# Kernel optimization log

Measured on AMD Instinct MI355X. Metric: run time of the kernel, lower is better.

The kernel has to match this reference:

```python
import jax, jax.numpy as jnp
import numpy as np

B, T, C, H = 4, 2048, 1024, 16
D = C // H  # head dim = 64


def setup_inputs() -> dict:
    key = jax.random.key(0)
    ks = jax.random.split(key, 5)
    s = 0.02
    return {
        "x": jax.random.normal(ks[0], (B, T, C), dtype=jnp.float32),
        "W_attn": jax.random.normal(ks[1], (C, 3 * C), dtype=jnp.float32) * s,
        "b_attn": jnp.zeros((3 * C,), dtype=jnp.float32),
        "W_proj": jax.random.normal(ks[2], (C, C), dtype=jnp.float32) * s,
        "b_proj": jnp.zeros((C,), dtype=jnp.float32),
    }


def reference(x, W_attn, b_attn, W_proj, b_proj):
    # qkv projection: [B,T,3C]
    qkv = x @ W_attn + b_attn
    q, k, v = jnp.split(qkv, 3, axis=-1)
    # [B,T,C] -> [B,H,T,D]
    def heads(t):
        return t.reshape(B, T, H, D).transpose(0, 2, 1, 3)
    q, k, v = heads(q), heads(k), heads(v)
    # scaled scores with causal mask, materialized [B,H,T,T] as in original
    att = jnp.einsum('bhqd,bhkd->bhqk', q, k) * (1.0 / np.sqrt(D))
    causal = jnp.tril(jnp.ones((T, T), dtype=bool))
    att = jnp.where(causal[None, None], att, -jnp.inf)
    att = jax.nn.softmax(att, axis=-1)
    y = jnp.einsum('bhqk,bhkd->bhqd', att, v)  # [B,H,T,D]
    y = y.transpose(0, 2, 1, 3).reshape(B, T, C)
    y = y @ W_proj + b_proj
    # original also returns present=(k,v); it is a pure pass-through cache
    return y
```

## Files before the change

kernel.cpp:

```cpp
#include <hip/hip_runtime.h>


typedef unsigned short u16;
typedef unsigned int u32;
typedef __attribute__((ext_vector_type(8))) unsigned short u16x8;
typedef __attribute__((ext_vector_type(4))) unsigned short u16x4;
typedef __attribute__((ext_vector_type(8))) short short8;
typedef __attribute__((ext_vector_type(4))) float f32x4;

__device__ inline u16 f2bf(float f) {
  unsigned u = __float_as_uint(f);
  u = (u + 0x7FFF + ((u >> 16) & 1)) >> 16;
  return (u16)u;
}

__device__ inline f32x4 mfma16(short8 a, short8 b, f32x4 c) {
  return __builtin_amdgcn_mfma_f32_16x16x32_bf16(a, b, c, 0, 0, 0);
}

__global__ __launch_bounds__(256) void k_cvt(const float* __restrict__ in,
                                             u16* __restrict__ out) {
  int i = (blockIdx.x * 256 + threadIdx.x) * 4;
  float4 v = *(const float4*)(in + i);
  u16x4 o = {f2bf(v.x), f2bf(v.y), f2bf(v.z), f2bf(v.w)};
  *(u16x4*)(out + i) = o;
}

__global__ __launch_bounds__(256) void k_tw(const float* __restrict__ in,
                                            u16* __restrict__ outT, int R, int Cc) {
  __shared__ u16 t[64][65];
  int c0 = blockIdx.x * 64, r0 = blockIdx.y * 64;
  int a = threadIdx.x & 63, w = threadIdx.x >> 6;
#pragma unroll
  for (int j = 0; j < 16; ++j) {
    int r = w + j * 4;
    t[r][a] = f2bf(in[(size_t)(r0 + r) * Cc + c0 + a]);
  }
  __syncthreads();
#pragma unroll
  for (int j = 0; j < 16; ++j) {
    int c = w + j * 4;
    outT[(size_t)(c0 + c) * R + r0 + a] = t[a][c];
  }
}

__global__ __launch_bounds__(256) void k_tv(const u16* __restrict__ qkv,
                                            u16* __restrict__ vt) {
  __shared__ u16 t[64][65];
  int t0 = blockIdx.x * 64, h = blockIdx.y, b = blockIdx.z;
  int a = threadIdx.x & 63, w = threadIdx.x >> 6;
#pragma unroll
  for (int j = 0; j < 16; ++j) {
    int tr = w + j * 4;
    t[tr][a] = qkv[(size_t)(b * 2048 + t0 + tr) * 3072 + 2048 + h * 64 + a];
  }
  __syncthreads();
#pragma unroll
  for (int j = 0; j < 16; ++j) {
    int d = w + j * 4;
    vt[((size_t)((b * 16 + h) * 64 + d)) * 2048 + t0 + a] = t[a][d];
  }
}

template <int OUTBF, int QSCALE>
__global__ __launch_bounds__(256) void gemm_bt(const u16* __restrict__ A,
                                               const u16* __restrict__ Bt,
                                               const float* __restrict__ bias,
                                               u16* __restrict__ outb,
                                               float* __restrict__ outf,
                                               int M, int N, int K) {
  __shared__ u16 As[128 * 64];
  __shared__ u16 Bs[128 * 64];
  const int m0 = blockIdx.x * 128, n0 = blockIdx.y * 128;
  const int tid = threadIdx.x, wave = tid >> 6, lane = tid & 63;
  const int quad = lane >> 4, l16 = lane & 15;
  const int wm = (wave & 1) * 64, wn = (wave >> 1) * 64;
  const int lrow = lane >> 3;
  const int lch = lane & 7;
  const int slot = lch ^ lrow;
  const u16* sA[4];
  const u16* sB[4];
  int offA[4], offB[4];
#pragma unroll
  for (int j = 0; j < 4; ++j) {
    int r = wave * 32 + j * 8;
    sA[j] = A + (size_t)(m0 + r + lrow) * K + lch * 8;
    sB[j] = Bt + (size_t)(n0 + r + lrow) * K + lch * 8;
    offA[j] = (r + lrow) * 64 + slot * 8;
    offB[j] = offA[j];
  }
  u16x8 ra[4], rb[4];
#pragma unroll
  for (int j = 0; j < 4; ++j) {
    ra[j] = *(const u16x8*)(sA[j]);
    rb[j] = *(const u16x8*)(sB[j]);
  }
  f32x4 acc[4][4] = {};
  for (int kt = 0; kt < K; kt += 64) {
    __syncthreads();
#pragma unroll
    for (int j = 0; j < 4; ++j) {
      *(u16x8*)&As[offA[j]] = ra[j];
      *(u16x8*)&Bs[offB[j]] = rb[j];
    }
    __syncthreads();
    if (kt + 64 < K) {
#pragma unroll
      for (int j = 0; j < 4; ++j) {
        ra[j] = *(const u16x8*)(sA[j] + kt + 64);
        rb[j] = *(const u16x8*)(sB[j] + kt + 64);
      }
    }
    const int sl = l16 & 7;
#pragma unroll
    for (int ks = 0; ks < 2; ++ks) {
      short8 af[4], bf[4];
#pragma unroll
      for (int mt = 0; mt < 4; ++mt)
        af[mt] = *(const short8*)(As + (wm + mt * 16 + l16) * 64 +
                                  ((ks * 4 + quad) ^ sl) * 8);
#pragma unroll
      for (int nt = 0; nt < 4; ++nt)
        bf[nt] = *(const short8*)(Bs + (wn + nt * 16 + l16) * 64 +
                                  ((ks * 4 + quad) ^ sl) * 8);
#pragma unroll
      for (int mt = 0; mt < 4; ++mt)
#pragma unroll
        for (int nt = 0; nt < 4; ++nt)
          acc[mt][nt] = mfma16(af[mt], bf[nt], acc[mt][nt]);
    }
  }
#pragma unroll
  for (int nt = 0; nt < 4; ++nt) {
    int col = n0 + wn + nt * 16 + l16;
    float bv = bias[col];
#pragma unroll
    for (int mt = 0; mt < 4; ++mt) {
      int rowb = m0 + wm + mt * 16 + quad * 4;
#pragma unroll
      for (int r = 0; r < 4; ++r) {
        float v = acc[mt][nt][r] + bv;
        if (QSCALE && col < 1024) v *= 0.18033688f;
        if (OUTBF)
          outb[(size_t)(rowb + r) * N + col] = f2bf(v);
        else
          outf[(size_t)(rowb + r) * N + col] = v;
      }
    }
  }
}

#define ATP 72
__global__ __launch_bounds__(256) void attn(const u16* __restrict__ qkv,
                                            const u16* __restrict__ vt,
                                            u16* __restrict__ y) {
  __shared__ u16 shm[256 * ATP];
  u16* Qs = shm;
  u16* Ks = shm + 128 * ATP;
  u16* Vs = shm + 192 * ATP;
  const int p = blockIdx.x, h = blockIdx.y, b = blockIdx.z;
  const int tid = threadIdx.x, wave = tid >> 6, lane = tid & 63;
  const int quad = lane >> 4, l16 = lane & 15;
  const u16* Qg = qkv + (size_t)b * 2048 * 3072 + h * 64;
  const u16* Kg = Qg + 1024;
  const u16* Vtg = vt + (size_t)(b * 16 + h) * 64 * 2048;
  const int srow0 = tid >> 3, scol0 = (tid & 7) * 8;
  u16* Pw0 = Qs + (wave * 16) * ATP;
  u16* Pw1 = Qs + (64 + wave * 16) * ATP;
  short8 ones_f;
#pragma unroll
  for (int j = 0; j < 8; ++j) ones_f[j] = 0x3F80;

  for (int half = 0; half < 2; ++half) {
    const int qb = half ? (15 - p) : p;
    const int q0 = qb * 128;
    const int nkt = 2 * qb + 2;
    const u16* kp0 = Kg + (size_t)srow0 * 3072 + scol0;
    const u16* kp1 = kp0 + 32 * 3072;
    const u16* vp0 = Vtg + (size_t)srow0 * 2048 + scol0;
    const u16* vp1 = vp0 + 32 * 2048;
    u16x8 qr0 = *(const u16x8*)(Qg + (size_t)(q0 + srow0) * 3072 + scol0);
    u16x8 qr1 = *(const u16x8*)(Qg + (size_t)(q0 + srow0 + 32) * 3072 + scol0);
    u16x8 qr2 = *(const u16x8*)(Qg + (size_t)(q0 + srow0 + 64) * 3072 + scol0);
    u16x8 qr3 = *(const u16x8*)(Qg + (size_t)(q0 + srow0 + 96) * 3072 + scol0);
    u16x8 kreg0 = *(const u16x8*)kp0, kreg1 = *(const u16x8*)kp1;
    u16x8 vreg0 = *(const u16x8*)vp0, vreg1 = *(const u16x8*)vp1;
    __syncthreads();
    *(u16x8*)&Qs[(size_t)srow0 * ATP + scol0] = qr0;
    *(u16x8*)&Qs[(size_t)(srow0 + 32) * ATP + scol0] = qr1;
    *(u16x8*)&Qs[(size_t)(srow0 + 64) * ATP + scol0] = qr2;
    *(u16x8*)&Qs[(size_t)(srow0 + 96) * ATP + scol0] = qr3;
    *(u16x8*)&Ks[(size_t)srow0 * ATP + scol0] = kreg0;
    *(u16x8*)&Ks[(size_t)(srow0 + 32) * ATP + scol0] = kreg1;
    *(u16x8*)&Vs[(size_t)srow0 * ATP + scol0] = vreg0;
    *(u16x8*)&Vs[(size_t)(srow0 + 32) * ATP + scol0] = vreg1;
    __syncthreads();
    short8 qf0a = *(const short8*)&Qs[(wave * 16 + l16) * ATP + quad * 8];
    short8 qf1a = *(const short8*)&Qs[(wave * 16 + l16) * ATP + 32 + quad * 8];
    short8 qf0b = *(const short8*)&Qs[(64 + wave * 16 + l16) * ATP + quad * 8];
    short8 qf1b = *(const short8*)&Qs[(64 + wave * 16 + l16) * ATP + 32 + quad * 8];

    f32x4 lacc0 = {}, lacc1 = {};
    f32x4 o0[4] = {}, o1[4] = {};

    auto tile = [&](int kt, int g0mode, bool g1mask) {
      if (kt > 0) {
        __syncthreads();
        *(u16x8*)&Ks[(size_t)srow0 * ATP + scol0] = kreg0;
        *(u16x8*)&Ks[(size_t)(srow0 + 32) * ATP + scol0] = kreg1;
        *(u16x8*)&Vs[(size_t)srow0 * ATP + scol0] = vreg0;
        *(u16x8*)&Vs[(size_t)(srow0 + 32) * ATP + scol0] = vreg1;
        __syncthreads();
      }
      if (kt + 1 < nkt) {
        kreg0 = *(const u16x8*)(kp0 += 64 * 3072);
        kreg1 = *(const u16x8*)(kp1 += 64 * 3072);
        vreg0 = *(const u16x8*)(vp0 += 64);
        vreg1 = *(const u16x8*)(vp1 += 64);
      }

      f32x4 s0[4] = {}, s1[4] = {};
#pragma unroll
      for (int mt = 0; mt < 4; ++mt) {
        short8 kf0 = *(const short8*)&Ks[(mt * 16 + l16) * ATP + quad * 8];
        short8 kf1 = *(const short8*)&Ks[(mt * 16 + l16) * ATP + 32 + quad * 8];
        if (g0mode < 2) {
          s0[mt] = mfma16(kf0, qf0a, s0[mt]);
          s0[mt] = mfma16(kf1, qf1a, s0[mt]);
        }
        s1[mt] = mfma16(kf0, qf0b, s1[mt]);
        s1[mt] = mfma16(kf1, qf1b, s1[mt]);
      }

      if (g0mode < 2) {
        const int qrow = q0 + wave * 16 + l16;
#pragma unroll
        for (int mt = 0; mt < 4; ++mt) {
          float pe[4];
#pragma unroll
          for (int r = 0; r < 4; ++r) {
            float pv = __builtin_amdgcn_exp2f(s0[mt][r]);
            if (g0mode == 1) {
              int kcol = kt * 64 + mt * 16 + quad * 4 + r;
              if (kcol > qrow) pv = 0.f;
            }
            pe[r] = pv;
          }
          u32 lo = __builtin_amdgcn_perm(__float_as_uint(pe[1]),
                                         __float_as_uint(pe[0]), 0x07060302u);
          u32 hi = __builtin_amdgcn_perm(__float_as_uint(pe[3]),
                                         __float_as_uint(pe[2]), 0x07060302u);
          uint2 pk = {lo, hi};
          *(uint2*)&Pw0[l16 * ATP + mt * 16 + quad * 4] = pk;
        }
      }
      {
        const int qrow = q0 + 64 + wave * 16 + l16;
#pragma unroll
        for (int mt = 0; mt < 4; ++mt) {
          float pe[4];
#pragma unroll
          for (int r = 0; r < 4; ++r) {
            float pv = __builtin_amdgcn_exp2f(s1[mt][r]);
            if (g1mask) {
              int kcol = kt * 64 + mt * 16 + quad * 4 + r;
              if (kcol > qrow) pv = 0.f;
            }
            pe[r] = pv;
          }
          u32 lo = __builtin_amdgcn_perm(__float_as_uint(pe[1]),
                                         __float_as_uint(pe[0]), 0x07060302u);
          u32 hi = __builtin_amdgcn_perm(__float_as_uint(pe[3]),
                                         __float_as_uint(pe[2]), 0x07060302u);
          uint2 pk = {lo, hi};
          *(uint2*)&Pw1[l16 * ATP + mt * 16 + quad * 4] = pk;
        }
      }

#pragma unroll
      for (int ks = 0; ks < 2; ++ks) {
        short8 pf0, pf1;
        if (g0mode < 2) {
          pf0 = *(const short8*)&Pw0[l16 * ATP + ks * 32 + quad * 8];
          lacc0 = mfma16(pf0, ones_f, lacc0);
        }
        pf1 = *(const short8*)&Pw1[l16 * ATP + ks * 32 + quad * 8];
        lacc1 = mfma16(pf1, ones_f, lacc1);
#pragma unroll
        for (int dt = 0; dt < 4; ++dt) {
          short8 vf = *(const short8*)&Vs[(dt * 16 + l16) * ATP + ks * 32 + quad * 8];
          if (g0mode < 2) o0[dt] = mfma16(pf0, vf, o0[dt]);
          o1[dt] = mfma16(pf1, vf, o1[dt]);
        }
      }
    };

    for (int kt = 0; kt < nkt - 2; ++kt) tile(kt, 0, false);
    tile(nkt - 2, 1, false);
    tile(nkt - 1, 2, true);

    size_t rb0 = (size_t)b * 2048 + q0 + wave * 16 + quad * 4;
#pragma unroll
    for (int r = 0; r < 4; ++r) {
      float inv = 1.f / lacc0[r];
#pragma unroll
      for (int dt = 0; dt < 4; ++dt)
        y[(rb0 + r) * 1024 + h * 64 + dt * 16 + l16] = f2bf(o0[dt][r] * inv);
    }
    size_t rb1 = rb0 + 64;
#pragma unroll
    for (int r = 0; r < 4; ++r) {
      float inv = 1.f / lacc1[r];
#pragma unroll
      for (int dt = 0; dt < 4; ++dt)
        y[(rb1 + r) * 1024 + h * 64 + dt * 16 + l16] = f2bf(o1[dt][r] * inv);
    }
  }
}

extern "C" void kernel_launch(void* const* d_in, const int* in_sizes, int n_in,
                              void* d_out, int out_size, void* d_ws, size_t ws_size,
                              hipStream_t stream) {
  const float* x = (const float*)d_in[0];
  const float* W_attn = (const float*)d_in[1];
  const float* b_attn = (const float*)d_in[2];
  const float* W_proj = (const float*)d_in[3];
  const float* b_proj = (const float*)d_in[4];
  float* out = (float*)d_out;
  char* ws = (char*)d_ws;
  u16* xb  = (u16*)(ws);
  u16* wta = (u16*)(ws + 16777216);
  u16* wtp = (u16*)(ws + 23068672);
  u16* qkv = (u16*)(ws + 25165824);
  u16* vt  = (u16*)(ws + 75497472);
  u16* y   = (u16*)(ws + 92274688);

  k_cvt<<<dim3(8192), 256, 0, stream>>>(x, xb);
  k_tw<<<dim3(48, 16), 256, 0, stream>>>(W_attn, wta, 1024, 3072);
  k_tw<<<dim3(16, 16), 256, 0, stream>>>(W_proj, wtp, 1024, 1024);
  gemm_bt<1, 1><<<dim3(64, 24), 256, 0, stream>>>(xb, wta, b_attn, qkv, nullptr, 8192, 3072, 1024);
  k_tv<<<dim3(32, 16, 4), 256, 0, stream>>>(qkv, vt);
  attn<<<dim3(8, 16, 4), 256, 0, stream>>>(qkv, vt, y);
  gemm_bt<0, 0><<<dim3(64, 8), 256, 0, stream>>>(y, wtp, b_proj, nullptr, out, 8192, 1024, 1024);
}
```

Before: 251.4 us.

## Replace QKV GEMM with 256x256 tile, 8-wave kernel using async LDS loads

Adds a new GEMM kernel for the QKV projection that uses 256x256 output tiles with 512 threads. It streams A and B directly into shared memory with global_load_lds through a 4-deep ring buffer, using swizzled columns to avoid LDS bank conflicts. MFMA phases are interleaved with barriers and priority raises. This targets global-to-LDS latency and register staging overhead and raises arithmetic intensity per tile. In exchange, the grid is smaller (384 blocks) and 128 KB of LDS per block limits occupancy, so tail effects could offset the gains.

```diff
diff --git a/kernel.cpp b/kernel.cpp
--- a/kernel.cpp
+++ b/kernel.cpp
@@ -18,6 +18,11 @@
   return __builtin_amdgcn_mfma_f32_16x16x32_bf16(a, b, c, 0, 0, 0);
 }
 
+__device__ __forceinline__ void gld16(const u16* g, u16* l) {
+  __builtin_amdgcn_global_load_lds((const __attribute__((address_space(1))) void*)g,
+                                   (__attribute__((address_space(3))) void*)l, 16, 0, 0);
+}
+
 __global__ __launch_bounds__(256) void k_cvt(const float* __restrict__ in,
                                              u16* __restrict__ out) {
   int i = (blockIdx.x * 256 + threadIdx.x) * 4;
@@ -59,6 +64,122 @@
   for (int j = 0; j < 16; ++j) {
     int d = w + j * 4;
     vt[((size_t)((b * 16 + h) * 64 + d)) * 2048 + t0 + a] = t[a][d];
+  }
+}
+
+template <int OUTBF, int QSCALE>
+__global__ __launch_bounds__(512, 2) void gemm256(const u16* __restrict__ A,
+                                                  const u16* __restrict__ Bt,
+                                                  const float* __restrict__ bias,
+                                                  u16* __restrict__ outb,
+                                                  float* __restrict__ outf,
+                                                  int M, int N, int K) {
+  __shared__ u16 As[4 * 8192];
+  __shared__ u16 Bs[4 * 8192];
+  const int m0 = blockIdx.x * 256, n0 = blockIdx.y * 256;
+  const int tid = threadIdx.x, wave = tid >> 6, lane = tid & 63;
+  const int quad = lane >> 4, l16 = lane & 15;
+  const int wm = wave >> 2, wn = wave & 3;
+  const int ns = K >> 5;
+
+  const int csw = (lane & 3) ^ ((lane >> 3) & 3);
+  const int srow = (wave * 2) * 16 + (lane >> 2);
+  const u16* gA0 = A + (size_t)(m0 + srow) * K + csw * 8;
+  const u16* gA1 = gA0 + (size_t)16 * K;
+  const u16* gB0 = Bt + (size_t)(n0 + srow) * K + csw * 8;
+  const u16* gB1 = gB0 + (size_t)16 * K;
+  u16* lA0 = &As[(wave * 2) * 512];
+  u16* lA1 = lA0 + 512;
+  u16* lB0 = &Bs[(wave * 2) * 512];
+  u16* lB1 = lB0 + 512;
+  const int slotq = quad ^ ((l16 >> 1) & 3);
+
+#define STAGE_A(s)                                  \
+  do {                                              \
+    int b_ = ((s) & 3) * 8192;                      \
+    gld16(gA0 + (size_t)(s) * 32, lA0 + b_);        \
+    gld16(gA1 + (size_t)(s) * 32, lA1 + b_);        \
+  } while (0)
+#define STAGE_B(s)                                  \
+  do {                                              \
+    int b_ = ((s) & 3) * 8192;                      \
+    gld16(gB0 + (size_t)(s) * 32, lB0 + b_);        \
+    gld16(gB1 + (size_t)(s) * 32, lB1 + b_);        \
+  } while (0)
+
+  f32x4 acc[8][4] = {};
+  STAGE_A(0); STAGE_B(0); STAGE_A(1); STAGE_B(1); STAGE_A(2); STAGE_B(2);
+  asm volatile("s_waitcnt vmcnt(8)" ::: "memory");
+  __builtin_amdgcn_s_barrier();
+
+#pragma unroll 4
+  for (int s = 0; s < ns; ++s) {
+    const u16* Ab = &As[(s & 3) * 8192];
+    const u16* Bb = &Bs[(s & 3) * 8192];
+    short8 bfr[4], af[4];
+#pragma unroll
+    for (int n = 0; n < 4; ++n)
+      bfr[n] = *(const short8*)&Bb[(wn * 64 + n * 16 + l16) * 32 + slotq * 8];
+#pragma unroll
+    for (int i = 0; i < 4; ++i)
+      af[i] = *(const short8*)&Ab[(wm * 128 + i * 16 + l16) * 32 + slotq * 8];
+    if (s + 3 < ns) STAGE_A(s + 3);
+    __builtin_amdgcn_sched_barrier(0);
+    __builtin_amdgcn_s_barrier();
+    asm volatile("s_waitcnt lgkmcnt(0)" ::: "memory");
+    __builtin_amdgcn_sched_barrier(0);
+    __builtin_amdgcn_s_setprio(1);
+#pragma unroll
+    for (int i = 0; i < 4; ++i)
+#pragma unroll
+      for (int n = 0; n < 4; ++n)
+        acc[i][n] = mfma16(af[i], bfr[n], acc[i][n]);
+    __builtin_amdgcn_s_setprio(0);
+    __builtin_amdgcn_sched_barrier(0);
+    __builtin_amdgcn_s_barrier();
+#pragma unroll
+    for (int i = 0; i < 4; ++i)
+      af[i] = *(const short8*)&Ab[(wm * 128 + 64 + i * 16 + l16) * 32 + slotq * 8];
+    if (s + 3 < ns) STAGE_B(s + 3);
+    if (s + 1 < ns) {
+      if (s + 3 < ns)      asm volatile("s_waitcnt vmcnt(8)" ::: "memory");
+      else if (s + 2 < ns) asm volatile("s_waitcnt vmcnt(4)" ::: "memory");
+      else                 asm volatile("s_waitcnt vmcnt(0)" ::: "memory");
+    }
+    __builtin_amdgcn_sched_barrier(0);
+    __builtin_amdgcn_s_barrier();
+    asm volatile("s_waitcnt lgkmcnt(0)" ::: "memory");
+    __builtin_amdgcn_sched_barrier(0);
+    __builtin_amdgcn_s_setprio(1);
+#pragma unroll
+    for (int i = 0; i < 4; ++i)
+#pragma unroll
+      for (int n = 0; n < 4; ++n)
+        acc[4 + i][n] = mfma16(af[i], bfr[n], acc[4 + i][n]);
+    __builtin_amdgcn_s_setprio(0);
+    __builtin_amdgcn_sched_barrier(0);
+    __builtin_amdgcn_s_barrier();
+  }
+#undef STAGE_A
+#undef STAGE_B
+
+#pragma unroll
+  for (int n = 0; n < 4; ++n) {
+    int col = n0 + wn * 64 + n * 16 + l16;
+    float bv = bias[col];
+#pragma unroll
+    for (int f = 0; f < 8; ++f) {
+      int rowb = m0 + wm * 128 + (f >> 2) * 64 + (f & 3) * 16 + quad * 4;
+#pragma unroll
+      for (int r = 0; r < 4; ++r) {
+        float v = acc[f][n][r] + bv;
+        if (QSCALE && col < 1024) v *= 0.18033688f;
+        if (OUTBF)
+          outb[(size_t)(rowb + r) * N + col] = f2bf(v);
+        else
+          outf[(size_t)(rowb + r) * N + col] = v;
+      }
+    }
   }
 }
 
@@ -338,7 +459,7 @@
   k_cvt<<<dim3(8192), 256, 0, stream>>>(x, xb);
   k_tw<<<dim3(48, 16), 256, 0, stream>>>(W_attn, wta, 1024, 3072);
   k_tw<<<dim3(16, 16), 256, 0, stream>>>(W_proj, wtp, 1024, 1024);
-  gemm_bt<1, 1><<<dim3(64, 24), 256, 0, stream>>>(xb, wta, b_attn, qkv, nullptr, 8192, 3072, 1024);
+  gemm256<1, 1><<<dim3(32, 12), 512, 0, stream>>>(xb, wta, b_attn, qkv, nullptr, 8192, 3072, 1024);
   k_tv<<<dim3(32, 16, 4), 256, 0, stream>>>(qkv, vt);
   attn<<<dim3(8, 16, 4), 256, 0, stream>>>(qkv, vt, y);
   gemm_bt<0, 0><<<dim3(64, 8), 256, 0, stream>>>(y, wtp, b_proj, nullptr, out, 8192, 1024, 1024);
```

Measured after the change: 265.8 us. 5.7% more time.
